# Optimization experiments

Hardware: AMD Instinct MI355X
Metric: run time of the kernel (lower is better)

## Reference

```python
import jax, jax.numpy as jnp
import numpy as np

N_NODES = 100000
N_EDGES = 400000
DIM = 128


def setup_inputs() -> dict:
    key = jax.random.key(0)
    ks = jax.random.split(key, 9)
    x = jax.random.normal(ks[0], (N_NODES, DIM), dtype=jnp.float32)
    edge_index3 = jax.random.randint(ks[1], (2, N_EDGES), 0, N_NODES, dtype=jnp.int64)
    edge_attr3 = jax.random.normal(ks[2], (N_EDGES, 16), dtype=jnp.float32)
    edge_attr4 = jax.random.normal(ks[3], (N_EDGES, 16), dtype=jnp.float32)
    batch = jnp.zeros((N_NODES,), dtype=jnp.int64)
    # torch Linear weights: [out_features, in_features]
    W1 = jax.random.normal(ks[4], (6 * DIM, 3 * DIM), dtype=jnp.float32) / np.sqrt(3 * DIM)
    b1 = jax.random.normal(ks[5], (6 * DIM,), dtype=jnp.float32) * 0.01
    W2 = jax.random.normal(ks[6], (1, 6 * DIM), dtype=jnp.float32) / np.sqrt(6 * DIM)
    b2 = jax.random.normal(ks[7], (1,), dtype=jnp.float32) * 0.01
    return {"x": x, "edge_index3": edge_index3, "edge_attr3": edge_attr3,
            "edge_attr4": edge_attr4, "batch": batch,
            "W1": W1, "b1": b1, "W2": W2, "b2": b2}


def reference(x, edge_index3, edge_attr3, edge_attr4, batch, W1, b1, W2, b2):
    # gather edge endpoint features: [E, DIM] each
    t0 = x[edge_index3[0]]
    t1 = x[edge_index3[1]]
    # mean over the 2 endpoints, elementwise product, squared difference -> [E, 3*DIM]
    feat = jnp.concatenate([(t0 + t1) * 0.5, t0 * t1, (t0 - t1) ** 2], axis=1)
    h = jax.nn.relu(feat @ W1.T + b1)          # [E, 6*DIM]
    yhat = (h @ W2.T + b2)[:, 0]               # [E]
    return yhat
```

## Files before the change

kernel.cpp:

```cpp
#include <hip/hip_runtime.h>

#define EDGES 400000
#define DIM 128

typedef __attribute__((ext_vector_type(8))) short bf16x8;
typedef __attribute__((ext_vector_type(4))) float f32x4;

__device__ __forceinline__ short f2bf(float f) {
    unsigned u = __builtin_bit_cast(unsigned, f);
    unsigned r = (u + 0x7fffu + ((u >> 16) & 1u)) >> 16;
    return (short)r;
}

__global__ void prep_w1(const float* __restrict__ W1, short* __restrict__ W1f) {
    int idx = blockIdx.x * 256 + threadIdx.x;
    int j    = idx & 7;
    int lane = (idx >> 3) & 63;
    int fs   = idx >> 9;
    int s    = fs % 12;
    int nt   = fs / 12;
    int n = nt * 16 + (lane & 15);
    int k = s * 32 + (lane >> 4) * 8 + j;
    W1f[idx] = f2bf(W1[n * 384 + k]);
}

__global__ __launch_bounds__(256, 2)
void edge_mlp(const float* __restrict__ x,
              const int*   __restrict__ ei,
              const float* __restrict__ b1,
              const float* __restrict__ W2,
              const float* __restrict__ b2p,
              const short* __restrict__ W1f,
              float* __restrict__ out)
{
    __shared__ short sB[2][12 * 512];

    const int tid  = threadIdx.x;
    const int lane = tid & 63;
    const int wave = tid >> 6;
    const int m    = lane & 15;
    const int quad = lane >> 4;
    const int eb   = blockIdx.x * 128;

    #pragma unroll
    for (int jj = 0; jj < 3; ++jj) {
        int s = wave * 3 + jj;
        __builtin_amdgcn_global_load_lds(
            (const __attribute__((address_space(1))) void*)(W1f + (s << 9) + lane * 8),
            (__attribute__((address_space(3))) void*)(&sB[0][s << 9]),
            16, 0, 0);
    }

    bf16x8 afrag[2][12];
    #pragma unroll
    for (int T = 0; T < 2; ++T) {
        int e = eb + wave * 32 + T * 16 + m;
        const float* r0 = x + (size_t)ei[e] * DIM;
        const float* r1 = x + (size_t)ei[EDGES + e] * DIM;
        #pragma unroll
        for (int i = 0; i < 4; ++i) {
            int c = i * 32 + quad * 8;
            float4 a0 = *(const float4*)(r0 + c);
            float4 a1 = *(const float4*)(r0 + c + 4);
            float4 c0 = *(const float4*)(r1 + c);
            float4 c1 = *(const float4*)(r1 + c + 4);
            float t0[8] = {a0.x,a0.y,a0.z,a0.w,a1.x,a1.y,a1.z,a1.w};
            float t1[8] = {c0.x,c0.y,c0.z,c0.w,c1.x,c1.y,c1.z,c1.w};
            bf16x8 fm, fp, fd;
            #pragma unroll
            for (int j = 0; j < 8; ++j) {
                float aa = t0[j], bb = t1[j];
                fm[j] = f2bf((aa + bb) * 0.5f);
                fp[j] = f2bf(aa * bb);
                float dd = aa - bb;
                fd[j] = f2bf(dd * dd);
            }
            afrag[T][i]     = fm;
            afrag[T][i + 4] = fp;
            afrag[T][i + 8] = fd;
        }
    }

    float yp0[4] = {0.f, 0.f, 0.f, 0.f};
    float yp1[4] = {0.f, 0.f, 0.f, 0.f};

    __syncthreads();

    for (int nt = 0; nt < 48; ++nt) {
        const int cur = nt & 1;

        if (nt + 1 < 48) {
            const short* src = W1f + (size_t)(nt + 1) * 6144;
            #pragma unroll
            for (int jj = 0; jj < 3; ++jj) {
                int s = wave * 3 + jj;
                __builtin_amdgcn_global_load_lds(
                    (const __attribute__((address_space(1))) void*)(src + (s << 9) + lane * 8),
                    (__attribute__((address_space(3))) void*)(&sB[cur ^ 1][s << 9]),
                    16, 0, 0);
            }
        }

        f32x4 acc0 = {0.f, 0.f, 0.f, 0.f};
        f32x4 acc1 = {0.f, 0.f, 0.f, 0.f};
        const bf16x8* bp = (const bf16x8*)sB[cur];
        #pragma unroll
        for (int s = 0; s < 12; ++s) {
            bf16x8 bfrag = bp[(s << 6) + lane];
            acc0 = __builtin_amdgcn_mfma_f32_16x16x32_bf16(afrag[0][s], bfrag, acc0, 0, 0, 0);
            acc1 = __builtin_amdgcn_mfma_f32_16x16x32_bf16(afrag[1][s], bfrag, acc1, 0, 0, 0);
        }

        int ng = nt * 16 + m;
        float bias = b1[ng];
        float w2v  = W2[ng];
        #pragma unroll
        for (int r = 0; r < 4; ++r) {
            float h0 = acc0[r] + bias;
            float h1 = acc1[r] + bias;
            yp0[r] = fmaf(fmaxf(h0, 0.f), w2v, yp0[r]);
            yp1[r] = fmaf(fmaxf(h1, 0.f), w2v, yp1[r]);
        }

        __syncthreads();
    }

    #pragma unroll
    for (int off = 8; off >= 1; off >>= 1) {
        #pragma unroll
        for (int r = 0; r < 4; ++r) {
            yp0[r] += __shfl_xor(yp0[r], off, 64);
            yp1[r] += __shfl_xor(yp1[r], off, 64);
        }
    }
    if (m == 0) {
        float b2v = b2p[0];
        int e0 = eb + wave * 32 + quad * 4;
        #pragma unroll
        for (int r = 0; r < 4; ++r) {
            out[e0 + r]      = yp0[r] + b2v;
            out[e0 + 16 + r] = yp1[r] + b2v;
        }
    }
}

extern "C" void kernel_launch(void* const* d_in, const int* in_sizes, int n_in,
                              void* d_out, int out_size, void* d_ws, size_t ws_size,
                              hipStream_t stream) {
    const float* x  = (const float*)d_in[0];
    const int*   ei = (const int*)  d_in[1];
    const float* W1 = (const float*)d_in[5];
    const float* b1 = (const float*)d_in[6];
    const float* W2 = (const float*)d_in[7];
    const float* b2 = (const float*)d_in[8];
    short* W1f = (short*)d_ws;
    float* out = (float*)d_out;

    prep_w1<<<1152, 256, 0, stream>>>(W1, W1f);
    edge_mlp<<<3125, 256, 0, stream>>>(x, ei, b1, W2, b2, W1f, out);
}
```

Before: 381.4 us.

## Give each wave 64 edges with 2 waves per block to reuse W1 tiles

Each block drops to 128 threads, and each wave now handles four 16-edge M-tiles instead of two. Every B fragment read from LDS therefore feeds four MFMAs, and each wave issues twice as many W1 tile loads. The intent is to halve LDS B-fragment traffic per MFMA and improve MFMA density. In exchange, register pressure roughly doubles for A fragments and accumulators (48 bf16x8 A fragments), which can cut occupancy or cause spills, and there are fewer waves per block to hide gather latency.

```diff
diff --git a/kernel.cpp b/kernel.cpp
--- a/kernel.cpp
+++ b/kernel.cpp
@@ -24,7 +24,7 @@
     W1f[idx] = f2bf(W1[n * 384 + k]);
 }
 
-__global__ __launch_bounds__(256, 2)
+__global__ __launch_bounds__(128, 2)
 void edge_mlp(const float* __restrict__ x,
               const int*   __restrict__ ei,
               const float* __restrict__ b1,
@@ -43,18 +43,18 @@
     const int eb   = blockIdx.x * 128;
 
     #pragma unroll
-    for (int jj = 0; jj < 3; ++jj) {
-        int s = wave * 3 + jj;
+    for (int jj = 0; jj < 6; ++jj) {
+        int s = wave * 6 + jj;
         __builtin_amdgcn_global_load_lds(
             (const __attribute__((address_space(1))) void*)(W1f + (s << 9) + lane * 8),
             (__attribute__((address_space(3))) void*)(&sB[0][s << 9]),
             16, 0, 0);
     }
 
-    bf16x8 afrag[2][12];
+    bf16x8 afrag[4][12];
     #pragma unroll
-    for (int T = 0; T < 2; ++T) {
-        int e = eb + wave * 32 + T * 16 + m;
+    for (int T = 0; T < 4; ++T) {
+        int e = eb + wave * 64 + T * 16 + m;
         const float* r0 = x + (size_t)ei[e] * DIM;
         const float* r1 = x + (size_t)ei[EDGES + e] * DIM;
         #pragma unroll
@@ -81,8 +81,11 @@
         }
     }
 
-    float yp0[4] = {0.f, 0.f, 0.f, 0.f};
-    float yp1[4] = {0.f, 0.f, 0.f, 0.f};
+    float yp[4][4];
+    #pragma unroll
+    for (int t = 0; t < 4; ++t)
+        #pragma unroll
+        for (int r = 0; r < 4; ++r) yp[t][r] = 0.f;
 
     __syncthreads();
 
@@ -92,8 +95,8 @@
         if (nt + 1 < 48) {
             const short* src = W1f + (size_t)(nt + 1) * 6144;
             #pragma unroll
-            for (int jj = 0; jj < 3; ++jj) {
-                int s = wave * 3 + jj;
+            for (int jj = 0; jj < 6; ++jj) {
+                int s = wave * 6 + jj;
                 __builtin_amdgcn_global_load_lds(
                     (const __attribute__((address_space(1))) void*)(src + (s << 9) + lane * 8),
                     (__attribute__((address_space(3))) void*)(&sB[cur ^ 1][s << 9]),
@@ -101,45 +104,47 @@
             }
         }
 
-        f32x4 acc0 = {0.f, 0.f, 0.f, 0.f};
-        f32x4 acc1 = {0.f, 0.f, 0.f, 0.f};
+        f32x4 acc[4];
+        #pragma unroll
+        for (int t = 0; t < 4; ++t) acc[t] = (f32x4){0.f, 0.f, 0.f, 0.f};
+
         const bf16x8* bp = (const bf16x8*)sB[cur];
         #pragma unroll
         for (int s = 0; s < 12; ++s) {
             bf16x8 bfrag = bp[(s << 6) + lane];
-            acc0 = __builtin_amdgcn_mfma_f32_16x16x32_bf16(afrag[0][s], bfrag, acc0, 0, 0, 0);
-            acc1 = __builtin_amdgcn_mfma_f32_16x16x32_bf16(afrag[1][s], bfrag, acc1, 0, 0, 0);
+            #pragma unroll
+            for (int t = 0; t < 4; ++t)
+                acc[t] = __builtin_amdgcn_mfma_f32_16x16x32_bf16(afrag[t][s], bfrag, acc[t], 0, 0, 0);
         }
 
         int ng = nt * 16 + m;
         float bias = b1[ng];
         float w2v  = W2[ng];
         #pragma unroll
-        for (int r = 0; r < 4; ++r) {
-            float h0 = acc0[r] + bias;
-            float h1 = acc1[r] + bias;
-            yp0[r] = fmaf(fmaxf(h0, 0.f), w2v, yp0[r]);
-            yp1[r] = fmaf(fmaxf(h1, 0.f), w2v, yp1[r]);
-        }
+        for (int t = 0; t < 4; ++t)
+            #pragma unroll
+            for (int r = 0; r < 4; ++r)
+                yp[t][r] = fmaf(fmaxf(acc[t][r] + bias, 0.f), w2v, yp[t][r]);
 
         __syncthreads();
     }
 
     #pragma unroll
-    for (int off = 8; off >= 1; off >>= 1) {
+    for (int off = 8; off >= 1; off >>= 1)
         #pragma unroll
-        for (int r = 0; r < 4; ++r) {
-            yp0[r] += __shfl_xor(yp0[r], off, 64);
-            yp1[r] += __shfl_xor(yp1[r], off, 64);
-        }
-    }
+        for (int t = 0; t < 4; ++t)
+            #pragma unroll
+            for (int r = 0; r < 4; ++r)
+                yp[t][r] += __shfl_xor(yp[t][r], off, 64);
+
     if (m == 0) {
         float b2v = b2p[0];
-        int e0 = eb + wave * 32 + quad * 4;
         #pragma unroll
-        for (int r = 0; r < 4; ++r) {
-            out[e0 + r]      = yp0[r] + b2v;
-            out[e0 + 16 + r] = yp1[r] + b2v;
+        for (int t = 0; t < 4; ++t) {
+            int e0 = eb + wave * 64 + t * 16 + quad * 4;
+            #pragma unroll
+            for (int r = 0; r < 4; ++r)
+                out[e0 + r] = yp[t][r] + b2v;
         }
     }
 }
@@ -157,5 +162,5 @@
     float* out = (float*)d_out;
 
     prep_w1<<<1152, 256, 0, stream>>>(W1, W1f);
-    edge_mlp<<<3125, 256, 0, stream>>>(x, ei, b1, W2, b2, W1f, out);
+    edge_mlp<<<3125, 128, 0, stream>>>(x, ei, b1, W2, b2, W1f, out);
 }
```

Result: slower. 609.0 us (+59.6%).

## Stream W1 fragments directly from global into registers, dropping LDS staging

Applied to the files above, without the earlier changes.

Replaces the LDS double-buffered staging of W1 tiles (async global-to-LDS loads plus a block barrier each step) with per-wave register double buffering that loads B fragments straight from global memory/L2. This removes the shared-memory round trip and the per-iteration __syncthreads. The cost is that every wave now fetches the full W1 independently, which raises cache traffic, and the extra 24 bf16x8 registers push register use up. Launch bounds are relaxed to one block per SM to allow that register growth, which may cut occupancy and weaken latency hiding for the edge gathers.

```diff
diff --git a/kernel.cpp b/kernel.cpp
--- a/kernel.cpp
+++ b/kernel.cpp
@@ -24,7 +24,7 @@
     W1f[idx] = f2bf(W1[n * 384 + k]);
 }
 
-__global__ __launch_bounds__(256, 2)
+__global__ __launch_bounds__(256, 1)
 void edge_mlp(const float* __restrict__ x,
               const int*   __restrict__ ei,
               const float* __restrict__ b1,
@@ -33,23 +33,12 @@
               const short* __restrict__ W1f,
               float* __restrict__ out)
 {
-    __shared__ short sB[2][12 * 512];
-
     const int tid  = threadIdx.x;
     const int lane = tid & 63;
     const int wave = tid >> 6;
     const int m    = lane & 15;
     const int quad = lane >> 4;
     const int eb   = blockIdx.x * 128;
-
-    #pragma unroll
-    for (int jj = 0; jj < 3; ++jj) {
-        int s = wave * 3 + jj;
-        __builtin_amdgcn_global_load_lds(
-            (const __attribute__((address_space(1))) void*)(W1f + (s << 9) + lane * 8),
-            (__attribute__((address_space(3))) void*)(&sB[0][s << 9]),
-            16, 0, 0);
-    }
 
     bf16x8 afrag[2][12];
     #pragma unroll
@@ -84,46 +73,49 @@
     float yp0[4] = {0.f, 0.f, 0.f, 0.f};
     float yp1[4] = {0.f, 0.f, 0.f, 0.f};
 
-    __syncthreads();
+    const bf16x8* __restrict__ bg = (const bf16x8*)W1f + lane;
 
-    for (int nt = 0; nt < 48; ++nt) {
-        const int cur = nt & 1;
+    bf16x8 bufA[12], bufB[12];
 
-        if (nt + 1 < 48) {
-            const short* src = W1f + (size_t)(nt + 1) * 6144;
-            #pragma unroll
-            for (int jj = 0; jj < 3; ++jj) {
-                int s = wave * 3 + jj;
-                __builtin_amdgcn_global_load_lds(
-                    (const __attribute__((address_space(1))) void*)(src + (s << 9) + lane * 8),
-                    (__attribute__((address_space(3))) void*)(&sB[cur ^ 1][s << 9]),
-                    16, 0, 0);
-            }
-        }
+    #pragma unroll
+    for (int s = 0; s < 12; ++s) bufA[s] = bg[s * 64];
+    #pragma unroll
+    for (int s = 0; s < 12; ++s) bufB[s] = bg[768 + s * 64];
 
-        f32x4 acc0 = {0.f, 0.f, 0.f, 0.f};
-        f32x4 acc1 = {0.f, 0.f, 0.f, 0.f};
-        const bf16x8* bp = (const bf16x8*)sB[cur];
-        #pragma unroll
-        for (int s = 0; s < 12; ++s) {
-            bf16x8 bfrag = bp[(s << 6) + lane];
-            acc0 = __builtin_amdgcn_mfma_f32_16x16x32_bf16(afrag[0][s], bfrag, acc0, 0, 0, 0);
-            acc1 = __builtin_amdgcn_mfma_f32_16x16x32_bf16(afrag[1][s], bfrag, acc1, 0, 0, 0);
-        }
+#define COMPUTE(buf, ntv)                                                     \
+    {                                                                         \
+        f32x4 acc0 = {0.f, 0.f, 0.f, 0.f};                                    \
+        f32x4 acc1 = {0.f, 0.f, 0.f, 0.f};                                    \
+        _Pragma("unroll")                                                     \
+        for (int s = 0; s < 12; ++s) {                                        \
+            acc0 = __builtin_amdgcn_mfma_f32_16x16x32_bf16(afrag[0][s], buf[s], acc0, 0, 0, 0); \
+            acc1 = __builtin_amdgcn_mfma_f32_16x16x32_bf16(afrag[1][s], buf[s], acc1, 0, 0, 0); \
+        }                                                                     \
+        int ng = (ntv) * 16 + m;                                              \
+        float bias = b1[ng];                                                  \
+        float w2v  = W2[ng];                                                  \
+        _Pragma("unroll")                                                     \
+        for (int r = 0; r < 4; ++r) {                                         \
+            yp0[r] = fmaf(fmaxf(acc0[r] + bias, 0.f), w2v, yp0[r]);           \
+            yp1[r] = fmaf(fmaxf(acc1[r] + bias, 0.f), w2v, yp1[r]);           \
+        }                                                                     \
+    }
 
-        int ng = nt * 16 + m;
-        float bias = b1[ng];
-        float w2v  = W2[ng];
-        #pragma unroll
-        for (int r = 0; r < 4; ++r) {
-            float h0 = acc0[r] + bias;
-            float h1 = acc1[r] + bias;
-            yp0[r] = fmaf(fmaxf(h0, 0.f), w2v, yp0[r]);
-            yp1[r] = fmaf(fmaxf(h1, 0.f), w2v, yp1[r]);
-        }
+#define LOADB(buf, ntv)                                                       \
+    {                                                                         \
+        const bf16x8* __restrict__ bp = bg + (size_t)(ntv) * 768;             \
+        _Pragma("unroll")                                                     \
+        for (int s = 0; s < 12; ++s) buf[s] = bp[s * 64];                     \
+    }
 
-        __syncthreads();
+    for (int nt = 0; nt < 48; nt += 2) {
+        COMPUTE(bufA, nt);
+        { int nn = (nt + 2 < 48) ? nt + 2 : 46; LOADB(bufA, nn); }
+        COMPUTE(bufB, nt + 1);
+        { int nn = (nt + 3 < 48) ? nt + 3 : 47; LOADB(bufB, nn); }
     }
+#undef COMPUTE
+#undef LOADB
 
     #pragma unroll
     for (int off = 8; off >= 1; off >>= 1) {
```

New measurement: 1.177 ms. 209% more time.
